# Kernel optimization log

Hardware: AMD Instinct MI355X
Metric: run time of the kernel (lower is better)

The kernel has to match this reference:

```python
import jax, jax.numpy as jnp
import numpy as np

N, E, T, D = 50000, 800000, 400000, 64


def _linear_params(key, fan_in, fan_out):
    kw, kb = jax.random.split(key)
    s = 1.0 / np.sqrt(fan_in)
    W = jax.random.uniform(kw, (fan_in, fan_out), minval=-s, maxval=s, dtype=jnp.float32)
    b = jax.random.uniform(kb, (fan_out,), minval=-s, maxval=s, dtype=jnp.float32)
    return W, b


def setup_inputs() -> dict:
    key = jax.random.key(0)
    ks = jax.random.split(key, 11)
    Ws1, bs1 = _linear_params(ks[0], 2 * D, D)
    Ws2, bs2 = _linear_params(ks[1], D, 3 * D)
    Wc1, bc1 = _linear_params(ks[2], 2 * D, D)
    Wc2, bc2 = _linear_params(ks[3], D, D)
    WV, bV = _linear_params(ks[4], D, D)
    return {
        "node_scalar": jax.random.normal(ks[5], (N, D), dtype=jnp.float32),
        "node_chiral": jax.random.normal(ks[6], (N, D), dtype=jnp.float32),
        "node_vector": jax.random.normal(ks[7], (N, 3, D), dtype=jnp.float32),
        "pos": jax.random.normal(ks[8], (N, 3), dtype=jnp.float32),
        "edge_index": jax.random.randint(ks[9], (E, 2), 0, N, dtype=jnp.int64),
        "triplet_index": jax.random.randint(ks[10], (T, 4), 0, N, dtype=jnp.int64),
        "Ws1": Ws1, "bs1": bs1, "Ws2": Ws2, "bs2": bs2,
        "Wc1": Wc1, "bc1": bc1, "Wc2": Wc2, "bc2": bc2,
        "WV": WV, "bV": bV,
    }


def reference(node_scalar, node_chiral, node_vector, pos, edge_index, triplet_index,
              Ws1, bs1, Ws2, bs2, Wc1, bc1, Wc2, bc2, WV, bV):
    n = node_scalar.shape[0]
    d = node_scalar.shape[1]
    e0, e1 = edge_index[:, 0], edge_index[:, 1]

    # Scalar / vector section: gather -> Linear-SiLU-Linear gate -> scatter-add
    g = jax.nn.silu(jnp.concatenate([node_scalar[e0], node_scalar[e1]], axis=1) @ Ws1 + bs1) @ Ws2 + bs2
    gate_vector, gate_edge, messages_ss = jnp.split(g, 3, axis=1)  # each [E, d]
    messages_vv = gate_vector[:, None, :] * node_vector[e1]               # [E, 3, d]
    rel = pos[e1] - pos[e0]                                               # [E, 3]
    messages_ev = gate_edge[:, None, :] * rel[:, :, None]                 # [E, 3, d]
    msg_ss = jax.ops.segment_sum(messages_ss, e0, num_segments=n)
    msg_vv = jax.ops.segment_sum(messages_vv, e0, num_segments=n)
    msg_ev = jax.ops.segment_sum(messages_ev, e0, num_segments=n)

    Vv = node_vector @ WV + bV          # [N, 3, d]
    Vv_norm = jnp.linalg.norm(Vv, axis=1)  # [N, d] (norm over spatial axis)
    message_vs = node_scalar * Vv_norm

    # Chiral section: triplet gathers, shared gate MLP, scalar triple product
    base, t1, t2, t3 = (triplet_index[:, i] for i in range(4))
    hc_base = node_chiral[base]

    def cgate(other):
        h = jnp.concatenate([hc_base, node_chiral[other]], axis=1)
        return jax.nn.silu(h @ Wc1 + bc1) @ Wc2 + bc2

    chiral_gate = cgate(t1) + cgate(t2) + cgate(t3)  # [T, d]
    pb = pos[base]
    r1, r2, r3 = pb - pos[t1], pb - pos[t2], pb - pos[t3]
    stp = jnp.einsum('ei,ei->e', r1, jnp.cross(r2, r3))  # scalar triple product [T]
    chiral_messages = chiral_gate / (stp + 0.01)[:, None]
    msg_chiral = jax.ops.segment_sum(chiral_messages, base, num_segments=n)

    return (node_scalar + msg_ss + message_vs,
            node_chiral + msg_chiral,
            node_vector + msg_vv + msg_ev)
```

## Files before the change

kernel.cpp:

```cpp
#include <hip/hip_runtime.h>
#include <math.h>

#define DD 64
typedef unsigned short ushort_t;
typedef __attribute__((ext_vector_type(8))) short bf16x8;
typedef __attribute__((ext_vector_type(4))) float f32x4;

__device__ __forceinline__ float silu_f(float x) {
    return x / (1.0f + __expf(-x));
}

__device__ __forceinline__ unsigned f32_to_bf16_rne(float x) {
    unsigned u = __float_as_uint(x);
    unsigned r = ((u >> 16) & 1u) + 0x7fffu;
    return (u + r) >> 16;
}

__device__ __forceinline__ float bf16_to_f32(ushort_t v) {
    return __uint_as_float(((unsigned)v) << 16);
}

__device__ __forceinline__ void gload_lds4(const void* gsrc, void* lds_base) {
    __builtin_amdgcn_global_load_lds(
        (const __attribute__((address_space(1))) void*)gsrc,
        (__attribute__((address_space(3))) void*)lds_base,
        4, 0, 0);
}

#define RFL(x) __builtin_amdgcn_readfirstlane(x)

__global__ __launch_bounds__(256) void hist_kernel(const int* __restrict__ eidx,
                                                   int* __restrict__ counts, int E) {
    int i = blockIdx.x * 256 + threadIdx.x;
    if (i < E) atomicAdd(&counts[((const int2*)eidx)[i].x], 1);
}

__global__ __launch_bounds__(1024) void scan_kernel(const int* __restrict__ counts,
                                                    int* __restrict__ cursor, int N) {
    __shared__ int part[1024];
    int tid = threadIdx.x;
    int CH = (N + 1023) / 1024;
    int lo = tid * CH, hi = lo + CH; if (hi > N) hi = N; if (lo > N) lo = N;
    int s = 0;
    for (int i = lo; i < hi; ++i) s += counts[i];
    part[tid] = s;
    __syncthreads();
    for (int d = 1; d < 1024; d <<= 1) {
        int v = (tid >= d) ? part[tid - d] : 0;
        __syncthreads();
        part[tid] += v;
        __syncthreads();
    }
    int run = (tid == 0) ? 0 : part[tid - 1];
    for (int i = lo; i < hi; ++i) {
        cursor[i] = run;
        run += counts[i];
    }
}

__global__ __launch_bounds__(256) void scatter2_kernel(const int* __restrict__ eidx,
                                                       const float* __restrict__ pos,
                                                       int* __restrict__ cursor,
                                                       int2* __restrict__ eperm,
                                                       float* __restrict__ relg, int E) {
    int i = blockIdx.x * 256 + threadIdx.x;
    if (i < E) {
        int2 p = ((const int2*)eidx)[i];
        int dst = atomicAdd(&cursor[p.x], 1);
        eperm[dst] = p;
        relg[3 * (size_t)dst + 0] = pos[(size_t)p.y * 3 + 0] - pos[(size_t)p.x * 3 + 0];
        relg[3 * (size_t)dst + 1] = pos[(size_t)p.y * 3 + 1] - pos[(size_t)p.x * 3 + 1];
        relg[3 * (size_t)dst + 2] = pos[(size_t)p.y * 3 + 2] - pos[(size_t)p.x * 3 + 2];
    }
}

__global__ __launch_bounds__(256) void node_transform_kernel(
    const float* __restrict__ ns, const float* __restrict__ nc,
    const float* __restrict__ Ws1, const float* __restrict__ Wc1,
    ushort_t* __restrict__ Abf, ushort_t* __restrict__ Bbf,
    float* __restrict__ C, float* __restrict__ Dm,
    float* __restrict__ out1, int N)
{
    __shared__ float w1[128 * 64];
    __shared__ float wc1s[128 * 64];
    __shared__ float xs[4][2][64];
    __shared__ float ys[4][2][64];
    int tid = threadIdx.x;
    for (int i = tid; i < 128 * 64 / 4; i += 256) {
        ((float4*)w1)[i]   = ((const float4*)Ws1)[i];
        ((float4*)wc1s)[i] = ((const float4*)Wc1)[i];
    }
    __syncthreads();
    int wave = tid >> 6, lane = tid & 63;
    for (int nb = blockIdx.x * 8; nb < N; nb += gridDim.x * 8) {
        int n0 = nb + wave * 2;
        #pragma unroll
        for (int s = 0; s < 2; ++s) {
            int n = n0 + s;
            float xv = 0.f, yv = 0.f;
            if (n < N) { xv = ns[(size_t)n * DD + lane]; yv = nc[(size_t)n * DD + lane]; }
            xs[wave][s][lane] = xv;
            ys[wave][s][lane] = yv;
        }
        float aA[2] = {0.f, 0.f}, aB[2] = {0.f, 0.f}, aC[2] = {0.f, 0.f}, aD[2] = {0.f, 0.f};
        for (int k = 0; k < 64; ++k) {
            float wa  = w1[k * 64 + lane];
            float wb  = w1[(64 + k) * 64 + lane];
            float wca = wc1s[k * 64 + lane];
            float wcb = wc1s[(64 + k) * 64 + lane];
            #pragma unroll
            for (int s = 0; s < 2; ++s) {
                float xk = xs[wave][s][k];
                float yk = ys[wave][s][k];
                aA[s] += xk * wa;  aB[s] += xk * wb;
                aC[s] += yk * wca; aD[s] += yk * wcb;
            }
        }
        #pragma unroll
        for (int s = 0; s < 2; ++s) {
            int n = n0 + s;
            if (n < N) {
                Abf[(size_t)n * DD + lane] = (ushort_t)f32_to_bf16_rne(aA[s]);
                Bbf[(size_t)n * DD + lane] = (ushort_t)f32_to_bf16_rne(aB[s]);
                C[(size_t)n * DD + lane]  = aC[s];
                Dm[(size_t)n * DD + lane] = aD[s];
                out1[(size_t)n * DD + lane] = ys[wave][s][lane];
            }
        }
    }
}

__global__ __launch_bounds__(256) void node_vector_kernel(
    const float* __restrict__ ns, const float* __restrict__ nv,
    const float* __restrict__ WV, const float* __restrict__ bV,
    float* __restrict__ out0, float* __restrict__ out2,
    ushort_t* __restrict__ nvbf, int N)
{
    __shared__ float wv[64 * 64];
    __shared__ float vs[4][2][3][64];
    int tid = threadIdx.x;
    for (int i = tid; i < 64 * 64 / 4; i += 256)
        ((float4*)wv)[i] = ((const float4*)WV)[i];
    __syncthreads();
    int wave = tid >> 6, lane = tid & 63;
    float bVj = bV[lane];
    for (int nb = blockIdx.x * 8; nb < N; nb += gridDim.x * 8) {
        int n0 = nb + wave * 2;
        #pragma unroll
        for (int s = 0; s < 2; ++s) {
            int n = n0 + s;
            float v0 = 0.f, v1 = 0.f, v2 = 0.f;
            if (n < N) {
                v0 = nv[((size_t)n * 3 + 0) * DD + lane];
                v1 = nv[((size_t)n * 3 + 1) * DD + lane];
                v2 = nv[((size_t)n * 3 + 2) * DD + lane];
            }
            vs[wave][s][0][lane] = v0; vs[wave][s][1][lane] = v1; vs[wave][s][2][lane] = v2;
        }
        float a0[2], a1[2], a2[2];
        #pragma unroll
        for (int s = 0; s < 2; ++s) { a0[s] = bVj; a1[s] = bVj; a2[s] = bVj; }
        for (int k = 0; k < 64; ++k) {
            float w = wv[k * 64 + lane];
            #pragma unroll
            for (int s = 0; s < 2; ++s) {
                a0[s] += vs[wave][s][0][k] * w;
                a1[s] += vs[wave][s][1][k] * w;
                a2[s] += vs[wave][s][2][k] * w;
            }
        }
        #pragma unroll
        for (int s = 0; s < 2; ++s) {
            int n = n0 + s;
            if (n < N) {
                float norm = sqrtf(a0[s] * a0[s] + a1[s] * a1[s] + a2[s] * a2[s]);
                float x = ns[(size_t)n * DD + lane];
                out0[(size_t)n * DD + lane] = x * (1.f + norm);
                float v0 = vs[wave][s][0][lane], v1 = vs[wave][s][1][lane], v2 = vs[wave][s][2][lane];
                out2[((size_t)n * 3 + 0) * DD + lane] = v0;
                out2[((size_t)n * 3 + 1) * DD + lane] = v1;
                out2[((size_t)n * 3 + 2) * DD + lane] = v2;
                nvbf[((size_t)n * 3 + 0) * DD + lane] = (ushort_t)f32_to_bf16_rne(v0);
                nvbf[((size_t)n * 3 + 1) * DD + lane] = (ushort_t)f32_to_bf16_rne(v1);
                nvbf[((size_t)n * 3 + 2) * DD + lane] = (ushort_t)f32_to_bf16_rne(v2);
            }
        }
    }
}

#define GEPW 16
__global__ __launch_bounds__(256) void edge_kernel(
    const ushort_t* __restrict__ Abf, const ushort_t* __restrict__ Bbf,
    const ushort_t* __restrict__ nvbf, const float* __restrict__ relg,
    const int2* __restrict__ eperm,
    const float* __restrict__ bs1, const float* __restrict__ Ws2, const float* __restrict__ bs2,
    float* __restrict__ out0, float* __restrict__ out2, int E)
{
    __shared__ unsigned w2frag[12 * 2 * 64 * 4];
    __shared__ ushort_t stAB[4][GEPW][128];
    __shared__ ushort_t stNV01[4][GEPW][132];
    __shared__ ushort_t stNV2[4][GEPW / 2][132];
    __shared__ float    relL[4][64];
    int tid = threadIdx.x;
    for (int i = tid; i < 12 * 2 * 64; i += 256) {
        int t  = i >> 7;
        int kk = (i >> 6) & 1;
        int l  = i & 63;
        int k0 = kk * 32 + (l >> 4) * 8;
        int col = t * 16 + (l & 15);
        #pragma unroll
        for (int jp = 0; jp < 4; ++jp) {
            float a = Ws2[(size_t)(k0 + 2 * jp) * 192 + col];
            float b = Ws2[(size_t)(k0 + 2 * jp + 1) * 192 + col];
            w2frag[i * 4 + jp] = f32_to_bf16_rne(a) | (f32_to_bf16_rne(b) << 16);
        }
    }
    __syncthreads();
    int wave = RFL(tid >> 6);
    int lane = tid & 63;
    float b1 = bs1[lane];
    float b2v_t[4], b2e_t[4], b2s_t[4];
    #pragma unroll
    for (int t = 0; t < 4; ++t) {
        b2v_t[t] = bs2[t * 16 + (lane & 15)];
        b2e_t[t] = bs2[64 + t * 16 + (lane & 15)];
        b2s_t[t] = bs2[128 + t * 16 + (lane & 15)];
    }

    int bid = blockIdx.x;
    int cpx = (int)(gridDim.x >> 3);
    int swz = (bid & 7) * cpx + (bid >> 3);

    long nG = ((long)E + GEPW - 1) / GEPW;
    for (long g = (long)swz * 4 + wave; g < nG; g += (long)gridDim.x * 4) {
        long e0b = g * GEPW;
        int i0a[GEPW], i1a[GEPW];
        #pragma unroll
        for (int e = 0; e < GEPW; ++e) {
            long eid = e0b + e; if (eid >= E) eid = E - 1;
            int2 p = eperm[eid];
            i0a[e] = RFL(p.x); i1a[e] = RFL(p.y);
        }
        #pragma unroll
        for (int e = 0; e < GEPW; ++e) {
            const char* srcAB = (lane < 32)
                ? ((const char*)Abf + (size_t)i0a[e] * 128 + lane * 4)
                : ((const char*)Bbf + (size_t)i1a[e] * 128 + (lane - 32) * 4);
            gload_lds4(srcAB, &stAB[wave][e][0]);
        }
        #pragma unroll
        for (int e = 0; e < GEPW; ++e)
            gload_lds4((const char*)nvbf + (size_t)i1a[e] * 384 + lane * 4, &stNV01[wave][e][0]);
        #pragma unroll
        for (int p2 = 0; p2 < GEPW / 2; ++p2) {
            const char* src2 = (lane < 32)
                ? ((const char*)nvbf + (size_t)i1a[2 * p2] * 384 + 256 + lane * 4)
                : ((const char*)nvbf + (size_t)i1a[2 * p2 + 1] * 384 + 256 + (lane - 32) * 4);
            gload_lds4(src2, &stNV2[wave][p2][0]);
        }
        gload_lds4((const char*)relg + e0b * 12 + lane * 4, &relL[wave][0]);
        asm volatile("s_waitcnt vmcnt(25)" ::: "memory");
        __builtin_amdgcn_sched_barrier(0);
        #pragma unroll
        for (int e = 0; e < GEPW; ++e) {
            float a = bf16_to_f32(stAB[wave][e][lane]);
            float b = bf16_to_f32(stAB[wave][e][64 + lane]);
            float h = silu_f(a + b + b1);
            *(float*)((char*)&stAB[wave][e][0] + ((lane * 4) ^ ((e & 7) << 5))) = h;
        }
        __builtin_amdgcn_sched_barrier(0);
        f32x4 acc[12];
        f32x4 zz = {0.f, 0.f, 0.f, 0.f};
        #pragma unroll
        for (int t = 0; t < 12; ++t) acc[t] = zz;
        int row = lane & 15;
        #pragma unroll
        for (int kk = 0; kk < 2; ++kk) {
            int coff = (kk * 128 + ((lane >> 4) * 32)) ^ ((row & 7) << 5);
            const char* hp = (const char*)&stAB[wave][row][0] + coff;
            float4 lo = *(const float4*)hp;
            float4 hi = *(const float4*)(hp + 16);
            unsigned a0, a1, a2, a3;
            asm("v_cvt_pk_bf16_f32 %0, %1, %2" : "=v"(a0) : "v"(lo.x), "v"(lo.y));
            asm("v_cvt_pk_bf16_f32 %0, %1, %2" : "=v"(a1) : "v"(lo.z), "v"(lo.w));
            asm("v_cvt_pk_bf16_f32 %0, %1, %2" : "=v"(a2) : "v"(hi.x), "v"(hi.y));
            asm("v_cvt_pk_bf16_f32 %0, %1, %2" : "=v"(a3) : "v"(hi.z), "v"(hi.w));
            union { unsigned u[4]; bf16x8 v; } af;
            af.u[0] = a0; af.u[1] = a1; af.u[2] = a2; af.u[3] = a3;
            #pragma unroll
            for (int t = 0; t < 12; ++t) {
                bf16x8 bf = *(const bf16x8*)&w2frag[((t * 2 + kk) * 64 + lane) * 4];
                acc[t] = __builtin_amdgcn_mfma_f32_16x16x32_bf16(af.v, bf, acc[t], 0, 0, 0);
            }
        }
        asm volatile("s_waitcnt vmcnt(0)" ::: "memory");
        __builtin_amdgcn_sched_barrier(0);
        int vi_all = 0;
        #pragma unroll
        for (int e = 0; e < GEPW; ++e) vi_all = (lane == e) ? i0a[e] : vi_all;
        int eLane0 = (lane >> 4) * 4;
        float aS[4]  = {0.f, 0.f, 0.f, 0.f};
        float aV0[4] = {0.f, 0.f, 0.f, 0.f};
        float aV1[4] = {0.f, 0.f, 0.f, 0.f};
        float aV2[4] = {0.f, 0.f, 0.f, 0.f};
        int icur = __builtin_amdgcn_ds_bpermute(eLane0 * 4, vi_all);
        #pragma unroll
        for (int rg = 0; rg < 4; ++rg) {
            int e = eLane0 + rg;
            int i0 = __builtin_amdgcn_ds_bpermute(e * 4, vi_all);
            bool ok = (e0b + e) < E;
            if (i0 != icur) {
                #pragma unroll
                for (int t = 0; t < 4; ++t) {
                    int dim = t * 16 + (lane & 15);
                    unsafeAtomicAdd(&out0[(size_t)(unsigned)icur * 64u + dim], aS[t]);
                    unsafeAtomicAdd(&out2[((size_t)(unsigned)icur * 3u + 0) * 64u + dim], aV0[t]);
                    unsafeAtomicAdd(&out2[((size_t)(unsigned)icur * 3u + 1) * 64u + dim], aV1[t]);
                    unsafeAtomicAdd(&out2[((size_t)(unsigned)icur * 3u + 2) * 64u + dim], aV2[t]);
                    aS[t] = 0.f; aV0[t] = 0.f; aV1[t] = 0.f; aV2[t] = 0.f;
                }
                icur = i0;
            }
            if (ok) {
                float r0v = relL[wave][e * 3 + 0];
                float r1v = relL[wave][e * 3 + 1];
                float r2v = relL[wave][e * 3 + 2];
                #pragma unroll
                for (int t = 0; t < 4; ++t) {
                    int dim = t * 16 + (lane & 15);
                    float gv = acc[t][rg]     + b2v_t[t];
                    float ge = acc[4 + t][rg] + b2e_t[t];
                    float ss = acc[8 + t][rg] + b2s_t[t];
                    float v0 = bf16_to_f32(stNV01[wave][e][dim]);
                    float v1 = bf16_to_f32(stNV01[wave][e][64 + dim]);
                    float v2 = bf16_to_f32(stNV2[wave][e >> 1][(e & 1) * 64 + dim]);
                    aS[t]  += ss;
                    aV0[t] += gv * v0 + ge * r0v;
                    aV1[t] += gv * v1 + ge * r1v;
                    aV2[t] += gv * v2 + ge * r2v;
                }
            }
        }
        #pragma unroll
        for (int t = 0; t < 4; ++t) {
            int dim = t * 16 + (lane & 15);
            unsafeAtomicAdd(&out0[(size_t)(unsigned)icur * 64u + dim], aS[t]);
            unsafeAtomicAdd(&out2[((size_t)(unsigned)icur * 3u + 0) * 64u + dim], aV0[t]);
            unsafeAtomicAdd(&out2[((size_t)(unsigned)icur * 3u + 1) * 64u + dim], aV1[t]);
            unsafeAtomicAdd(&out2[((size_t)(unsigned)icur * 3u + 2) * 64u + dim], aV2[t]);
        }
    }
}

#define TPW 4
__global__ __launch_bounds__(256) void triplet_kernel(
    const float* __restrict__ C, const float* __restrict__ Dm,
    const float* __restrict__ pos, const int* __restrict__ tidx,
    const float* __restrict__ bc1, const float* __restrict__ Wc2, const float* __restrict__ bc2,
    float* __restrict__ out1, int T)
{
    __shared__ float wT[64 * 64];
    __shared__ float stC[4][TPW][64];
    __shared__ float stD[4][TPW][3][64];
    int tid = threadIdx.x;
    for (int i = tid; i < 64 * 64 / 4; i += 256)
        ((float4*)wT)[i] = ((const float4*)Wc2)[i];
    __syncthreads();
    int wave = RFL(tid >> 6);
    int lane = tid & 63;
    float b1 = bc1[lane];
    float b2 = bc2[lane] * 3.0f;
    for (long bb = (long)blockIdx.x * (4 * TPW); bb < T; bb += (long)gridDim.x * (4 * TPW)) {
        long t0 = bb + wave * TPW;
        int ib[TPW], it1[TPW], it2[TPW], it3[TPW];
        #pragma unroll
        for (int e = 0; e < TPW; ++e) {
            long t = t0 + e;
            int b = 0, t1 = 0, t2 = 0, t3 = 0;
            if (t < T) { int4 q = ((const int4*)tidx)[t]; b = q.x; t1 = q.y; t2 = q.z; t3 = q.w; }
            ib[e]  = RFL(b);
            it1[e] = RFL(t1);
            it2[e] = RFL(t2);
            it3[e] = RFL(t3);
        }
        #pragma unroll
        for (int e = 0; e < TPW; ++e) {
            gload_lds4(C  + (size_t)ib[e]  * DD + lane, &stC[wave][e][0]);
            gload_lds4(Dm + (size_t)it1[e] * DD + lane, &stD[wave][e][0][0]);
            gload_lds4(Dm + (size_t)it2[e] * DD + lane, &stD[wave][e][1][0]);
            gload_lds4(Dm + (size_t)it3[e] * DD + lane, &stD[wave][e][2][0]);
        }
        asm volatile("s_waitcnt vmcnt(0)" ::: "memory");
        float inv[TPW];
        #pragma unroll
        for (int e = 0; e < TPW; ++e) {
            float hb = stC[wave][e][lane] + b1;
            float h = silu_f(hb + stD[wave][e][0][lane])
                    + silu_f(hb + stD[wave][e][1][lane])
                    + silu_f(hb + stD[wave][e][2][lane]);
            stC[wave][e][lane] = h;
            int b = ib[e], t1 = it1[e], t2 = it2[e], t3 = it3[e];
            double pbx = pos[(size_t)b * 3], pby = pos[(size_t)b * 3 + 1], pbz = pos[(size_t)b * 3 + 2];
            double r1x = pbx - pos[(size_t)t1 * 3], r1y = pby - pos[(size_t)t1 * 3 + 1], r1z = pbz - pos[(size_t)t1 * 3 + 2];
            double r2x = pbx - pos[(size_t)t2 * 3], r2y = pby - pos[(size_t)t2 * 3 + 1], r2z = pbz - pos[(size_t)t2 * 3 + 2];
            double r3x = pbx - pos[(size_t)t3 * 3], r3y = pby - pos[(size_t)t3 * 3 + 1], r3z = pbz - pos[(size_t)t3 * 3 + 2];
            double cx = r2y * r3z - r2z * r3y;
            double cy = r2z * r3x - r2x * r3z;
            double cz = r2x * r3y - r2y * r3x;
            double stp = r1x * cx + r1y * cy + r1z * cz;
            inv[e] = (float)(1.0 / (stp + 0.01));
        }
        float acc[TPW];
        #pragma unroll
        for (int e = 0; e < TPW; ++e) acc[e] = 0.f;
        for (int k4 = 0; k4 < 64; k4 += 4) {
            float4 hk[TPW];
            #pragma unroll
            for (int e = 0; e < TPW; ++e) hk[e] = *(const float4*)&stC[wave][e][k4];
            #pragma unroll
            for (int kk = 0; kk < 4; ++kk) {
                float wk = wT[(k4 + kk) * 64 + lane];
                #pragma unroll
                for (int e = 0; e < TPW; ++e) acc[e] += (&hk[e].x)[kk] * wk;
            }
        }
        #pragma unroll
        for (int e = 0; e < TPW; ++e) {
            long t = t0 + e;
            if (t >= T) break;
            unsafeAtomicAdd(&out1[(size_t)ib[e] * DD + lane], (acc[e] + b2) * inv[e]);
        }
    }
}

extern "C" void kernel_launch(void* const* d_in, const int* in_sizes, int n_in,
                              void* d_out, int out_size, void* d_ws, size_t ws_size,
                              hipStream_t stream)
{
    const float* ns  = (const float*)d_in[0];
    const float* nc  = (const float*)d_in[1];
    const float* nv  = (const float*)d_in[2];
    const float* pos = (const float*)d_in[3];
    const int* eidx  = (const int*)d_in[4];
    const int* tidx  = (const int*)d_in[5];
    const float* Ws1 = (const float*)d_in[6];
    const float* bs1 = (const float*)d_in[7];
    const float* Ws2 = (const float*)d_in[8];
    const float* bs2 = (const float*)d_in[9];
    const float* Wc1 = (const float*)d_in[10];
    const float* bc1 = (const float*)d_in[11];
    const float* Wc2 = (const float*)d_in[12];
    const float* bc2 = (const float*)d_in[13];
    const float* WV  = (const float*)d_in[14];
    const float* bV  = (const float*)d_in[15];

    int N = in_sizes[0] / 64;
    int E = in_sizes[4] / 2;
    int T = in_sizes[5] / 4;

    float* out0 = (float*)d_out;
    float* out1 = out0 + (size_t)N * 64;
    float* out2 = out1 + (size_t)N * 64;

    float* C    = (float*)d_ws;
    float* Dm   = C + (size_t)N * 64;
    float* relg = Dm + (size_t)N * 64;
    int2* eperm = (int2*)(relg + (size_t)E * 3 + 64);
    int* counts = (int*)(eperm + (size_t)E);
    int* cursor = counts + N;
    ushort_t* Abf  = (ushort_t*)(cursor + N);
    ushort_t* Bbf  = Abf + (size_t)N * 64;
    ushort_t* nvbf = Bbf + (size_t)N * 64;

    hipMemsetAsync(counts, 0, (size_t)N * sizeof(int), stream);
    hist_kernel<<<(E + 255) / 256, 256, 0, stream>>>(eidx, counts, E);
    scan_kernel<<<1, 1024, 0, stream>>>(counts, cursor, N);
    scatter2_kernel<<<(E + 255) / 256, 256, 0, stream>>>(eidx, pos, cursor, eperm, relg, E);
    node_transform_kernel<<<2048, 256, 0, stream>>>(ns, nc, Ws1, Wc1, Abf, Bbf, C, Dm, out1, N);
    node_vector_kernel<<<2048, 256, 0, stream>>>(ns, nv, WV, bV, out0, out2, nvbf, N);
    edge_kernel<<<4096, 256, 0, stream>>>(Abf, Bbf, nvbf, relg, eperm, bs1, Ws2, bs2, out0, out2, E);
    triplet_kernel<<<4096, 256, 0, stream>>>(C, Dm, pos, tidx, bc1, Wc2, bc2, out1, T);
}
```

Baseline: 951.7 us.

## Pack node-vector x/y bf16 pairs and load directly into registers in edge kernel

Splits the bf16 node-vector buffer into a packed (v0,v1) uint32 array and a separate v2 bf16 array. The edge kernel now loads the v0/v1 pair straight into registers in the MFMA output layout (via bpermute of the destination index), which removes the stNV01 LDS staging and its reads. Separately, the triplet kernel processes 8 triplets per wave and launches half as many blocks. The cost is more outstanding register loads during the MFMA phase and a different waitcnt accounting, which could change latency hiding.

```diff
diff --git a/kernel.cpp b/kernel.cpp
--- a/kernel.cpp
+++ b/kernel.cpp
@@ -18,6 +18,10 @@
 
 __device__ __forceinline__ float bf16_to_f32(ushort_t v) {
     return __uint_as_float(((unsigned)v) << 16);
+}
+
+__device__ __forceinline__ float2 bf2_lo_hi(unsigned u) {
+    return make_float2(__uint_as_float(u << 16), __uint_as_float(u & 0xffff0000u));
 }
 
 __device__ __forceinline__ void gload_lds4(const void* gsrc, void* lds_base) {
@@ -134,7 +138,7 @@
     const float* __restrict__ ns, const float* __restrict__ nv,
     const float* __restrict__ WV, const float* __restrict__ bV,
     float* __restrict__ out0, float* __restrict__ out2,
-    ushort_t* __restrict__ nvbf, int N)
+    unsigned* __restrict__ nv01p, ushort_t* __restrict__ nv2bf, int N)
 {
     __shared__ float wv[64 * 64];
     __shared__ float vs[4][2][3][64];
@@ -180,9 +184,8 @@
                 out2[((size_t)n * 3 + 0) * DD + lane] = v0;
                 out2[((size_t)n * 3 + 1) * DD + lane] = v1;
                 out2[((size_t)n * 3 + 2) * DD + lane] = v2;
-                nvbf[((size_t)n * 3 + 0) * DD + lane] = (ushort_t)f32_to_bf16_rne(v0);
-                nvbf[((size_t)n * 3 + 1) * DD + lane] = (ushort_t)f32_to_bf16_rne(v1);
-                nvbf[((size_t)n * 3 + 2) * DD + lane] = (ushort_t)f32_to_bf16_rne(v2);
+                nv01p[(size_t)n * DD + lane] = f32_to_bf16_rne(v0) | (f32_to_bf16_rne(v1) << 16);
+                nv2bf[(size_t)n * DD + lane] = (ushort_t)f32_to_bf16_rne(v2);
             }
         }
     }
@@ -191,14 +194,13 @@
 #define GEPW 16
 __global__ __launch_bounds__(256) void edge_kernel(
     const ushort_t* __restrict__ Abf, const ushort_t* __restrict__ Bbf,
-    const ushort_t* __restrict__ nvbf, const float* __restrict__ relg,
-    const int2* __restrict__ eperm,
+    const unsigned* __restrict__ nv01p, const ushort_t* __restrict__ nv2bf,
+    const float* __restrict__ relg, const int2* __restrict__ eperm,
     const float* __restrict__ bs1, const float* __restrict__ Ws2, const float* __restrict__ bs2,
     float* __restrict__ out0, float* __restrict__ out2, int E)
 {
     __shared__ unsigned w2frag[12 * 2 * 64 * 4];
     __shared__ ushort_t stAB[4][GEPW][128];
-    __shared__ ushort_t stNV01[4][GEPW][132];
     __shared__ ushort_t stNV2[4][GEPW / 2][132];
     __shared__ float    relL[4][64];
     int tid = threadIdx.x;
@@ -241,6 +243,12 @@
             int2 p = eperm[eid];
             i0a[e] = RFL(p.x); i1a[e] = RFL(p.y);
         }
+        int vi_all = 0, vi1_all = 0;
+        #pragma unroll
+        for (int e = 0; e < GEPW; ++e) {
+            vi_all  = (lane == e) ? i0a[e] : vi_all;
+            vi1_all = (lane == e) ? i1a[e] : vi1_all;
+        }
         #pragma unroll
         for (int e = 0; e < GEPW; ++e) {
             const char* srcAB = (lane < 32)
@@ -248,17 +256,27 @@
                 : ((const char*)Bbf + (size_t)i1a[e] * 128 + (lane - 32) * 4);
             gload_lds4(srcAB, &stAB[wave][e][0]);
         }
-        #pragma unroll
-        for (int e = 0; e < GEPW; ++e)
-            gload_lds4((const char*)nvbf + (size_t)i1a[e] * 384 + lane * 4, &stNV01[wave][e][0]);
+        __builtin_amdgcn_sched_barrier(0);
         #pragma unroll
         for (int p2 = 0; p2 < GEPW / 2; ++p2) {
             const char* src2 = (lane < 32)
-                ? ((const char*)nvbf + (size_t)i1a[2 * p2] * 384 + 256 + lane * 4)
-                : ((const char*)nvbf + (size_t)i1a[2 * p2 + 1] * 384 + 256 + (lane - 32) * 4);
+                ? ((const char*)nv2bf + (size_t)i1a[2 * p2] * 128 + lane * 4)
+                : ((const char*)nv2bf + (size_t)i1a[2 * p2 + 1] * 128 + (lane - 32) * 4);
             gload_lds4(src2, &stNV2[wave][p2][0]);
         }
         gload_lds4((const char*)relg + e0b * 12 + lane * 4, &relL[wave][0]);
+        int eL0 = (lane >> 4) * 4;
+        unsigned nv01r[4][4];
+        #pragma unroll
+        for (int rg = 0; rg < 4; ++rg) {
+            int i1s = __builtin_amdgcn_ds_bpermute((eL0 + rg) * 4, vi1_all);
+            const char* basep = (const char*)nv01p + (size_t)(unsigned)i1s * 256 + (lane & 15) * 4;
+            nv01r[rg][0] = *(const unsigned*)(basep);
+            nv01r[rg][1] = *(const unsigned*)(basep + 64);
+            nv01r[rg][2] = *(const unsigned*)(basep + 128);
+            nv01r[rg][3] = *(const unsigned*)(basep + 192);
+        }
+        __builtin_amdgcn_sched_barrier(0);
         asm volatile("s_waitcnt vmcnt(25)" ::: "memory");
         __builtin_amdgcn_sched_barrier(0);
         #pragma unroll
@@ -295,18 +313,14 @@
         }
         asm volatile("s_waitcnt vmcnt(0)" ::: "memory");
         __builtin_amdgcn_sched_barrier(0);
-        int vi_all = 0;
-        #pragma unroll
-        for (int e = 0; e < GEPW; ++e) vi_all = (lane == e) ? i0a[e] : vi_all;
-        int eLane0 = (lane >> 4) * 4;
         float aS[4]  = {0.f, 0.f, 0.f, 0.f};
         float aV0[4] = {0.f, 0.f, 0.f, 0.f};
         float aV1[4] = {0.f, 0.f, 0.f, 0.f};
         float aV2[4] = {0.f, 0.f, 0.f, 0.f};
-        int icur = __builtin_amdgcn_ds_bpermute(eLane0 * 4, vi_all);
+        int icur = __builtin_amdgcn_ds_bpermute(eL0 * 4, vi_all);
         #pragma unroll
         for (int rg = 0; rg < 4; ++rg) {
-            int e = eLane0 + rg;
+            int e = eL0 + rg;
             int i0 = __builtin_amdgcn_ds_bpermute(e * 4, vi_all);
             bool ok = (e0b + e) < E;
             if (i0 != icur) {
@@ -331,13 +345,12 @@
                     float gv = acc[t][rg]     + b2v_t[t];
                     float ge = acc[4 + t][rg] + b2e_t[t];
                     float ss = acc[8 + t][rg] + b2s_t[t];
-                    float v0 = bf16_to_f32(stNV01[wave][e][dim]);
-                    float v1 = bf16_to_f32(stNV01[wave][e][64 + dim]);
+                    float2 vv = bf2_lo_hi(nv01r[rg][t]);
                     float v2 = bf16_to_f32(stNV2[wave][e >> 1][(e & 1) * 64 + dim]);
                     aS[t]  += ss;
-                    aV0[t] += gv * v0 + ge * r0v;
-                    aV1[t] += gv * v1 + ge * r1v;
-                    aV2[t] += gv * v2 + ge * r2v;
+                    aV0[t] += gv * vv.x + ge * r0v;
+                    aV1[t] += gv * vv.y + ge * r1v;
+                    aV2[t] += gv * v2   + ge * r2v;
                 }
             }
         }
@@ -352,7 +365,7 @@
     }
 }
 
-#define TPW 4
+#define TPW 8
 __global__ __launch_bounds__(256) void triplet_kernel(
     const float* __restrict__ C, const float* __restrict__ Dm,
     const float* __restrict__ pos, const int* __restrict__ tidx,
@@ -468,16 +481,17 @@
     int2* eperm = (int2*)(relg + (size_t)E * 3 + 64);
     int* counts = (int*)(eperm + (size_t)E);
     int* cursor = counts + N;
-    ushort_t* Abf  = (ushort_t*)(cursor + N);
-    ushort_t* Bbf  = Abf + (size_t)N * 64;
-    ushort_t* nvbf = Bbf + (size_t)N * 64;
+    unsigned* nv01p = (unsigned*)(cursor + N);
+    ushort_t* Abf   = (ushort_t*)(nv01p + (size_t)N * 64);
+    ushort_t* Bbf   = Abf + (size_t)N * 64;
+    ushort_t* nv2bf = Bbf + (size_t)N * 64;
 
     hipMemsetAsync(counts, 0, (size_t)N * sizeof(int), stream);
     hist_kernel<<<(E + 255) / 256, 256, 0, stream>>>(eidx, counts, E);
     scan_kernel<<<1, 1024, 0, stream>>>(counts, cursor, N);
     scatter2_kernel<<<(E + 255) / 256, 256, 0, stream>>>(eidx, pos, cursor, eperm, relg, E);
     node_transform_kernel<<<2048, 256, 0, stream>>>(ns, nc, Ws1, Wc1, Abf, Bbf, C, Dm, out1, N);
-    node_vector_kernel<<<2048, 256, 0, stream>>>(ns, nv, WV, bV, out0, out2, nvbf, N);
-    edge_kernel<<<4096, 256, 0, stream>>>(Abf, Bbf, nvbf, relg, eperm, bs1, Ws2, bs2, out0, out2, E);
-    triplet_kernel<<<4096, 256, 0, stream>>>(C, Dm, pos, tidx, bc1, Wc2, bc2, out1, T);
-}
+    node_vector_kernel<<<2048, 256, 0, stream>>>(ns, nv, WV, bV, out0, out2, nv01p, nv2bf, N);
+    edge_kernel<<<4096, 256, 0, stream>>>(Abf, Bbf, nv01p, nv2bf, relg, eperm, bs1, Ws2, bs2, out0, out2, E);
+    triplet_kernel<<<2048, 256, 0, stream>>>(C, Dm, pos, tidx, bc1, Wc2, bc2, out1, T);
+}
```

After: 953.6 us. Within noise of the previous version (+0.2%).
